# Kernel tuning notes

Measured on AMD Instinct MI355X. Metric: run time of the kernel, lower is better.

The kernel has to match this reference:

```python
import jax, jax.numpy as jnp
import numpy as np

# ---- hyperparameters (from init_kwargs) ----
W_KL = 1.0
W_AUX = 0.1
W_TRANS = 0.5
KL_FREE_BITS = 0.5
DIST_GAMMA = 1.0
FOCAL_GAMMA = 2.0
FOCAL_ALPHA = 0.6
SDTW_GAMMA = 0.1
BANDWIDTH = 150
BIG = 1e8  # finite 'infinity' so softmin gradients stay nan-free


def _focal_manhattan_cost(x, y):
    """Pairwise focal-weighted Manhattan distance.
    x: (B,N,D), y: (B,M,D) -> (B,N,M).
    d = dist_gamma * L1(x_i, y_j); focal weight alpha*(1-exp(-d))**focal_gamma.
    """
    d = DIST_GAMMA * jnp.abs(x[:, :, None, :] - y[:, None, :, :]).sum(-1)  # (B,N,M)
    w = FOCAL_ALPHA * (1.0 - jnp.exp(-d)) ** FOCAL_GAMMA
    return w * d


def _soft_dtw(x, y):
    """Banded Soft-DTW via anti-diagonal wavefront scan. x,y: (B,T,D) -> (B,)."""
    C = _focal_manhattan_cost(x, y)  # (B,T,T)
    B, T, _ = C.shape
    ii = jnp.arange(T + 1)  # padded row index i in [0,T]

    def _shift(a):  # a[:, i] -> a[:, i-1], pad with BIG
        return jnp.concatenate([jnp.full((a.shape[0], 1), BIG, a.dtype), a[:, :-1]], axis=1)

    def step(carry, d):
        prev2, prev = carry  # diagonals d-2, d-1; shape (B, T+1) indexed by i
        jj = d - ii
        valid = (ii >= 1) & (ii <= T) & (jj >= 1) & (jj <= T) & (jnp.abs(ii - jj) <= BANDWIDTH)
        ci = jnp.clip(ii - 1, 0, T - 1)
        cj = jnp.clip(jj - 1, 0, T - 1)
        cost = C[:, ci, cj]                     # (B, T+1) diagonal of cost matrix
        up = _shift(prev)                        # R[i-1, j]
        left = prev                              # R[i, j-1]
        diag = _shift(prev2)                     # R[i-1, j-1]
        stacked = jnp.stack([up, left, diag])    # (3, B, T+1)
        smin = -SDTW_GAMMA * jax.nn.logsumexp(stacked / (-SDTW_GAMMA), axis=0)
        r = jnp.where(valid, cost + smin, BIG)
        return (prev, r), None

    # d=0 diagonal: R[0,0]=0; d=1 diagonal: all boundary = BIG
    prev2 = jnp.full((B, T + 1), BIG, C.dtype).at[:, 0].set(0.0)
    prev = jnp.full((B, T + 1), BIG, C.dtype)
    (_, last), _ = jax.lax.scan(step, (prev2, prev), jnp.arange(2, 2 * T + 1))
    return last[:, T]  # R[T,T]


def _loss(pred_traj, ground_truth, style_mu, style_logvar, pred_trans_count, perm_gen, perm_real):
    # NAG loss: average Hausdorff (symmetric soft-DTW) + variation term
    sim = _soft_dtw(pred_traj, ground_truth).mean() + _soft_dtw(ground_truth, pred_traj).mean()
    d_gen = _soft_dtw(pred_traj, pred_traj[perm_gen]).mean()
    d_real = _soft_dtw(ground_truth, ground_truth[perm_real]).mean()
    nag = sim + jnp.abs(d_gen - d_real)

    # KL with free bits
    kl_div = -0.5 * jnp.sum(1.0 + style_logvar - style_mu ** 2 - jnp.exp(style_logvar), axis=1)
    kl = jnp.maximum(kl_div - KL_FREE_BITS, 0.0).mean()

    # transition counts
    gt_touch = ground_truth[..., 2]
    gt_trans = jnp.abs(gt_touch[:, 1:] - gt_touch[:, :-1]).sum(axis=1)  # hard count
    aux = jnp.mean((pred_trans_count.squeeze(-1) - gt_trans) ** 2)
    sharp = jax.nn.sigmoid((pred_traj[..., 2] - 0.5) * 10.0)
    pred_trans_soft = jnp.abs(sharp[:, 1:] - sharp[:, :-1]).sum(axis=1)
    trans_reg = jnp.mean((pred_trans_soft - gt_trans) ** 2)

    total = nag + W_KL * kl + W_AUX * aux + W_TRANS * trans_reg
    return total, nag, kl, aux, trans_reg


def setup_inputs() -> dict:
    key = jax.random.key(0)
    ks = jax.random.split(key, 7)
    B, T, D, L = 128, 256, 3, 128
    return {
        "pred_traj": jax.random.uniform(ks[0], (B, T, D), jnp.float32),
        "ground_truth": jax.random.uniform(ks[1], (B, T, D), jnp.float32),
        "style_mu": jax.random.normal(ks[2], (B, L), jnp.float32),
        "style_logvar": jax.random.normal(ks[3], (B, L), jnp.float32),
        "pred_trans_count": jax.random.normal(ks[4], (B, 1), jnp.float32),
        "perm_gen": jax.random.permutation(ks[5], B),
        "perm_real": jax.random.permutation(ks[6], B),
    }


def reference(pred_traj, ground_truth, style_mu, style_logvar, pred_trans_count, perm_gen, perm_real):
    return _loss(pred_traj, ground_truth, style_mu, style_logvar, pred_trans_count, perm_gen, perm_real)
```

## Files before the change

### kernel.cpp

```cpp
#include <hip/hip_runtime.h>

#define Tn 256
#define UBIG (-1.442695e9f)
#define CBIG (-3.0e9f)
#define E2(v)  __builtin_amdgcn_exp2f(v)

__global__ __launch_bounds__(256) void sdtw_kernel(
    const float* __restrict__ pred, const float* __restrict__ gt,
    const float* __restrict__ mu, const float* __restrict__ lv,
    const float* __restrict__ ptc,
    const int* __restrict__ perm_gen, const int* __restrict__ perm_real,
    float* __restrict__ ws) {
  __shared__ float ylds[Tn][3];
  __shared__ float rng[3][512];
  __shared__ volatile int prog[4];
  __shared__ float red[256];
  __shared__ float gtr_sh;

  const int t = threadIdx.x;

  if (blockIdx.x >= 384) {
    const int b = blockIdx.x - 384;

    float v = 0.0f;
    if (t < 128) {
      const float m = mu[b * 128 + t];
      const float l = lv[b * 128 + t];
      v = 1.0f + l - m * m - E2(l * 1.44269504f);
    }
    red[t] = v; __syncthreads();
    for (int s = 128; s > 0; s >>= 1) { if (t < s) red[t] += red[t + s]; __syncthreads(); }
    if (t == 0) ws[512 + b] = fmaxf(-0.5f * red[0] - 0.5f, 0.0f);
    __syncthreads();

    float g = 0.0f;
    if (t < Tn - 1)
      g = fabsf(gt[(b * Tn + t + 1) * 3 + 2] - gt[(b * Tn + t) * 3 + 2]);
    red[t] = g; __syncthreads();
    for (int s = 128; s > 0; s >>= 1) { if (t < s) red[t] += red[t + s]; __syncthreads(); }
    if (t == 0) gtr_sh = red[0];
    __syncthreads();
    const float gtr = gtr_sh;

    float p = 0.0f;
    if (t < Tn - 1) {
      const float q0 = pred[(b * Tn + t) * 3 + 2];
      const float q1 = pred[(b * Tn + t + 1) * 3 + 2];
      const float s0 = __builtin_amdgcn_rcpf(1.f + E2((q0 - 0.5f) * -14.4269504f));
      const float s1 = __builtin_amdgcn_rcpf(1.f + E2((q1 - 0.5f) * -14.4269504f));
      p = fabsf(s1 - s0);
    }
    red[t] = p; __syncthreads();
    for (int s = 128; s > 0; s >>= 1) { if (t < s) red[t] += red[t + s]; __syncthreads(); }
    if (t == 0) {
      const float pts = red[0];
      const float d1 = ptc[b] - gtr; ws[640 + b] = d1 * d1;
      const float d2 = pts - gtr;    ws[768 + b] = d2 * d2;
    }
    return;
  }

  const int blk = blockIdx.x;
  const int c = blk >> 7;
  const int b = blk & 127;

  const float* x;
  const float* y;
  if (c == 0)      { x = pred + b * Tn * 3; y = gt   + b * Tn * 3; }
  else if (c == 1) { x = pred + b * Tn * 3; y = pred + perm_gen[b]  * Tn * 3; }
  else             { x = gt   + b * Tn * 3; y = gt   + perm_real[b] * Tn * 3; }

  const int w = t >> 6;
  const int lane = t & 63;
  float* rngf = (float*)&rng[0][0];

  if (w == 0)      __builtin_amdgcn_s_setprio(3);
  else if (w == 1) __builtin_amdgcn_s_setprio(2);
  else if (w == 2) __builtin_amdgcn_s_setprio(1);

  for (int k = t; k < Tn * 3; k += 256) (&ylds[0][0])[k] = y[k] * 1.44269504f;
  for (int k = t; k < 3 * 512; k += 256) rngf[k] = UBIG;
  if (t < 4) prog[t] = 0;

  const float x0 = x[t * 3 + 0] * 1.44269504f;
  const float x1 = x[t * 3 + 1] * 1.44269504f;
  const float x2 = x[t * 3 + 2] * 1.44269504f;

  const int i = t + 1;
  const int lo = max(i + 1, 2 * i - 150);
  const int hi = min(i + Tn, 2 * i + 150);
  const unsigned span = (unsigned)(hi - lo);

  const int dstart = (w == 0) ? 2 : (w == 1) ? 66 : (w == 2) ? 130 : 225;
  const int dend   = (w == 0) ? 290 : (w == 1) ? 386 : (w == 2) ? 450 : 513;
  const bool wlt3 = (w != 3);

  int cjb = dstart - t - 2;
  int vdb = dstart - lo;

  __syncthreads();

  float lf = UBIG;
  float dgv;
  if (w > 0) {
    const int need0 = dstart - 2;
    int pv = prog[w - 1];
    while (pv < need0) { __builtin_amdgcn_s_sleep(1); pv = prog[w - 1]; }
    int gi = (w - 1) * 512 + dstart - 2;
    __asm__ volatile("" : "+v"(gi) : "v"(pv));
    const float r0 = rngf[gi];
    dgv = (lane == 0) ? r0 : UBIG;
  } else {
    dgv = (lane == 0) ? 0.0f : UBIG;
  }

#define COSTV(IDX, VD) ({                                                \
    const int cj_ = (IDX) & 255;                                         \
    const float a0 = x0 - ylds[cj_][0];                                  \
    const float a1 = x1 - ylds[cj_][1];                                  \
    const float a2 = x2 - ylds[cj_][2];                                  \
    const float dl_ = fabsf(a0) + fabsf(a1) + fabsf(a2);                 \
    const float om_ = 1.0f - E2(-dl_);                                   \
    const float cv_ = fmaf(om_ * dl_, -6.0f * om_, -127.0f);             \
    ((unsigned)(VD) <= span) ? cv_ : CBIG; })

  float cc[16], cn[16];
  #pragma unroll
  for (int k = 0; k < 16; ++k) cc[k] = COSTV(cjb + k, vdb + k);

  for (int dbase = dstart; dbase < dend; dbase += 16) {
    float bb[16];
    if (w > 0) {
      const int need = dbase + 14;
      int pv = prog[w - 1];
      while (pv < need) { __builtin_amdgcn_s_sleep(1); pv = prog[w - 1]; }
      int gb = (w - 1) * 512 + dbase - 1;
      __asm__ volatile("" : "+v"(gb) : "v"(pv));
      #pragma unroll
      for (int k = 0; k < 16; ++k) bb[k] = rngf[gb + k];
    } else {
      #pragma unroll
      for (int k = 0; k < 16; ++k) bb[k] = UBIG;
    }

    float rr[16];
    #pragma unroll
    for (int k = 0; k < 16; ++k) {
      const float upv = __int_as_float(__builtin_amdgcn_update_dpp(
          __float_as_int(bb[k]), __float_as_int(lf),
          0x138 , 0xf, 0xf, false));

      const float mx = fmaxf(fmaxf(upv, lf), dgv);
      const float md = __builtin_amdgcn_fmed3f(upv, lf, dgv);
      const float mn = fminf(fminf(upv, lf), dgv);
      const float fa = fmaf(md - mx, 8388608.0f, 1065353216.0f);
      const float fb = fmaf(mn - mx, 8388608.0f, 1065353216.0f);
      int ia, ib;
      __asm__("v_cvt_i32_f32 %0, %1" : "=v"(ia) : "v"(fa));
      __asm__("v_cvt_i32_f32 %0, %1" : "=v"(ib) : "v"(fb));
      const float s  = 1.0f + __int_as_float(ia) + __int_as_float(ib);
      const float fs = (float)__float_as_int(s);
      const float un = fmaf(fs, 1.1920928955e-7f, mx + cc[k]);
      rr[k] = un;
      dgv = upv;
      lf = un;
    }

    if (wlt3 && lane == 63) {
      #pragma unroll
      for (int k = 0; k < 16; ++k) rngf[w * 512 + dbase + k] = rr[k];
      prog[w] = dbase + 15;
    }

    #pragma unroll
    for (int k = 0; k < 16; ++k) cn[k] = COSTV(cjb + 16 + k, vdb + 16 + k);

    #pragma unroll
    for (int k = 0; k < 16; ++k) cc[k] = cn[k];
    cjb += 16;
    vdb += 16;
  }

  if (wlt3 && lane == 63) prog[w] = 0x7fffffff;

  if (t == 255) ws[blk] = lf * -0.0693147181f;
#undef COSTV
}

__global__ __launch_bounds__(128) void final_kernel(
    const float* __restrict__ ws, float* __restrict__ out) {
  const int t = threadIdx.x;
  __shared__ float red[128];
  const int offs[6] = {0, 128, 256, 512, 640, 768};
  float sums[6];
  #pragma unroll
  for (int q = 0; q < 6; ++q) {
    red[t] = ws[offs[q] + t];
    __syncthreads();
    for (int s = 64; s > 0; s >>= 1) { if (t < s) red[t] += red[t + s]; __syncthreads(); }
    if (t == 0) sums[q] = red[0];
    __syncthreads();
  }
  if (t == 0) {
    const float inv = 1.0f / 128.0f;
    const float sim   = 2.0f * sums[0] * inv;
    const float dgen  = sums[1] * inv;
    const float dreal = sums[2] * inv;
    const float nag   = sim + fabsf(dgen - dreal);
    const float kl    = sums[3] * inv;
    const float aux   = sums[4] * inv;
    const float trans = sums[5] * inv;
    const float total = nag + 1.0f * kl + 0.1f * aux + 0.5f * trans;
    out[0] = total;
    out[1] = nag;
    out[2] = kl;
    out[3] = aux;
    out[4] = trans;
  }
}

extern "C" void kernel_launch(void* const* d_in, const int* in_sizes, int n_in,
                              void* d_out, int out_size, void* d_ws, size_t ws_size,
                              hipStream_t stream) {
  const float* pred = (const float*)d_in[0];
  const float* gt   = (const float*)d_in[1];
  const float* mu   = (const float*)d_in[2];
  const float* lv   = (const float*)d_in[3];
  const float* ptc  = (const float*)d_in[4];
  const int*   pg   = (const int*)d_in[5];
  const int*   pr   = (const int*)d_in[6];
  float* ws  = (float*)d_ws;
  float* out = (float*)d_out;

  sdtw_kernel<<<512, 256, 0, stream>>>(pred, gt, mu, lv, ptc, pg, pr, ws);
  final_kernel<<<1, 128, 0, stream>>>(ws, out);
}
```

Before: 79.45 us.

## Double-buffer wavefront boundary loads and cost prefetch, use float4 LDS layout

Measured after the change: 70.77 us (median of 2 runs). -10.9%, faster.

```diff
diff --git a/kernel.cpp b/kernel.cpp
--- a/kernel.cpp
+++ b/kernel.cpp
@@ -4,6 +4,7 @@
 #define UBIG (-1.442695e9f)
 #define CBIG (-3.0e9f)
 #define E2(v)  __builtin_amdgcn_exp2f(v)
+#define L2E 1.44269504f
 
 __global__ __launch_bounds__(256) void sdtw_kernel(
     const float* __restrict__ pred, const float* __restrict__ gt,
@@ -11,8 +12,8 @@
     const float* __restrict__ ptc,
     const int* __restrict__ perm_gen, const int* __restrict__ perm_real,
     float* __restrict__ ws) {
-  __shared__ float ylds[Tn][3];
-  __shared__ float rng[3][512];
+  __shared__ float4 ylds4[640];
+  __shared__ float rng[3][520];
   __shared__ volatile int prog[4];
   __shared__ float red[256];
   __shared__ float gtr_sh;
@@ -26,7 +27,7 @@
     if (t < 128) {
       const float m = mu[b * 128 + t];
       const float l = lv[b * 128 + t];
-      v = 1.0f + l - m * m - E2(l * 1.44269504f);
+      v = 1.0f + l - m * m - E2(l * L2E);
     }
     red[t] = v; __syncthreads();
     for (int s = 128; s > 0; s >>= 1) { if (t < s) red[t] += red[t + s]; __syncthreads(); }
@@ -78,113 +79,129 @@
   else if (w == 1) __builtin_amdgcn_s_setprio(2);
   else if (w == 2) __builtin_amdgcn_s_setprio(1);
 
-  for (int k = t; k < Tn * 3; k += 256) (&ylds[0][0])[k] = y[k] * 1.44269504f;
-  for (int k = t; k < 3 * 512; k += 256) rngf[k] = UBIG;
+  for (int k = t; k < 640; k += 256) {
+    const int row = (k & 255) * 3;
+    ylds4[k] = float4{y[row] * L2E, y[row + 1] * L2E, y[row + 2] * L2E, 0.f};
+  }
+  for (int k = t; k < 3 * 520; k += 256) rngf[k] = UBIG;
   if (t < 4) prog[t] = 0;
 
-  const float x0 = x[t * 3 + 0] * 1.44269504f;
-  const float x1 = x[t * 3 + 1] * 1.44269504f;
-  const float x2 = x[t * 3 + 2] * 1.44269504f;
+  const float x0 = x[t * 3 + 0] * L2E;
+  const float x1 = x[t * 3 + 1] * L2E;
+  const float x2 = x[t * 3 + 2] * L2E;
 
   const int i = t + 1;
   const int lo = max(i + 1, 2 * i - 150);
   const int hi = min(i + Tn, 2 * i + 150);
   const unsigned span = (unsigned)(hi - lo);
 
-  const int dstart = (w == 0) ? 2 : (w == 1) ? 66 : (w == 2) ? 130 : 225;
-  const int dend   = (w == 0) ? 290 : (w == 1) ? 386 : (w == 2) ? 450 : 513;
+  const int dstart = (w == 0) ? 2 : (w == 1) ? 66 : (w == 2) ? 130 : 226;
+  const int dend   = (w == 0) ? 290 : (w == 1) ? 386 : (w == 2) ? 450 : 514;
   const bool wlt3 = (w != 3);
-
-  int cjb = dstart - t - 2;
-  int vdb = dstart - lo;
 
   __syncthreads();
 
   float lf = UBIG;
   float dgv;
+  float bbA[16], bbB[16], ccA[16], ccB[16];
+  int pvn = 0;
+
   if (w > 0) {
-    const int need0 = dstart - 2;
+    const int need0 = dstart + 14;
     int pv = prog[w - 1];
     while (pv < need0) { __builtin_amdgcn_s_sleep(1); pv = prog[w - 1]; }
-    int gi = (w - 1) * 512 + dstart - 2;
-    __asm__ volatile("" : "+v"(gi) : "v"(pv));
-    const float r0 = rngf[gi];
+    int gb = (w - 1) * 520 + dstart - 2;
+    __asm__ volatile("" : "+v"(gb) : "v"(pv));
+    const float r0 = rngf[gb];
     dgv = (lane == 0) ? r0 : UBIG;
+    #pragma unroll
+    for (int k = 0; k < 16; ++k) bbA[k] = rngf[gb + 1 + k];
+    pvn = prog[w - 1];
   } else {
     dgv = (lane == 0) ? 0.0f : UBIG;
-  }
-
-#define COSTV(IDX, VD) ({                                                \
-    const int cj_ = (IDX) & 255;                                         \
-    const float a0 = x0 - ylds[cj_][0];                                  \
-    const float a1 = x1 - ylds[cj_][1];                                  \
-    const float a2 = x2 - ylds[cj_][2];                                  \
-    const float dl_ = fabsf(a0) + fabsf(a1) + fabsf(a2);                 \
-    const float om_ = 1.0f - E2(-dl_);                                   \
-    const float cv_ = fmaf(om_ * dl_, -6.0f * om_, -127.0f);             \
-    ((unsigned)(VD) <= span) ? cv_ : CBIG; })
-
-  float cc[16], cn[16];
-  #pragma unroll
-  for (int k = 0; k < 16; ++k) cc[k] = COSTV(cjb + k, vdb + k);
-
-  for (int dbase = dstart; dbase < dend; dbase += 16) {
-    float bb[16];
-    if (w > 0) {
-      const int need = dbase + 14;
-      int pv = prog[w - 1];
-      while (pv < need) { __builtin_amdgcn_s_sleep(1); pv = prog[w - 1]; }
-      int gb = (w - 1) * 512 + dbase - 1;
-      __asm__ volatile("" : "+v"(gb) : "v"(pv));
-      #pragma unroll
-      for (int k = 0; k < 16; ++k) bb[k] = rngf[gb + k];
-    } else {
-      #pragma unroll
-      for (int k = 0; k < 16; ++k) bb[k] = UBIG;
-    }
-
-    float rr[16];
     #pragma unroll
-    for (int k = 0; k < 16; ++k) {
-      const float upv = __int_as_float(__builtin_amdgcn_update_dpp(
-          __float_as_int(bb[k]), __float_as_int(lf),
-          0x138 , 0xf, 0xf, false));
-
-      const float mx = fmaxf(fmaxf(upv, lf), dgv);
-      const float md = __builtin_amdgcn_fmed3f(upv, lf, dgv);
-      const float mn = fminf(fminf(upv, lf), dgv);
-      const float fa = fmaf(md - mx, 8388608.0f, 1065353216.0f);
-      const float fb = fmaf(mn - mx, 8388608.0f, 1065353216.0f);
-      int ia, ib;
-      __asm__("v_cvt_i32_f32 %0, %1" : "=v"(ia) : "v"(fa));
-      __asm__("v_cvt_i32_f32 %0, %1" : "=v"(ib) : "v"(fb));
-      const float s  = 1.0f + __int_as_float(ia) + __int_as_float(ib);
-      const float fs = (float)__float_as_int(s);
-      const float un = fmaf(fs, 1.1920928955e-7f, mx + cc[k]);
-      rr[k] = un;
-      dgv = upv;
-      lf = un;
-    }
-
-    if (wlt3 && lane == 63) {
-      #pragma unroll
-      for (int k = 0; k < 16; ++k) rngf[w * 512 + dbase + k] = rr[k];
-      prog[w] = dbase + 15;
-    }
-
-    #pragma unroll
-    for (int k = 0; k < 16; ++k) cn[k] = COSTV(cjb + 16 + k, vdb + 16 + k);
-
-    #pragma unroll
-    for (int k = 0; k < 16; ++k) cc[k] = cn[k];
-    cjb += 16;
-    vdb += 16;
+    for (int k = 0; k < 16; ++k) { bbA[k] = UBIG; bbB[k] = UBIG; }
+  }
+
+#define PREF16(CCX, DB) do {                                               \
+    const int sb_ = (DB) - t + 254;                                        \
+    const int vd_ = (DB) - lo;                                             \
+    _Pragma("unroll")                                                      \
+    for (int k_ = 0; k_ < 16; ++k_) {                                      \
+      const float4 yv_ = ylds4[sb_ + k_];                                  \
+      const float dl_ = fabsf(x0 - yv_.x) + fabsf(x1 - yv_.y) + fabsf(x2 - yv_.z); \
+      const float ef_ = fmaf(dl_, -8388608.f, 1065353216.f);               \
+      const float e_  = __int_as_float((int)ef_);                          \
+      const float om_ = 1.f - e_;                                          \
+      const float cv_ = fmaf(om_ * dl_, -6.f * om_, -127.f);               \
+      CCX[k_] = ((unsigned)(vd_ + k_) <= span) ? cv_ : CBIG;               \
+    } } while (0)
+
+#define CORE16(BBX, CCX, DB) do {                                          \
+    float rr_[16];                                                         \
+    _Pragma("unroll")                                                      \
+    for (int k_ = 0; k_ < 16; ++k_) {                                      \
+      const float upv_ = __int_as_float(__builtin_amdgcn_update_dpp(       \
+          __float_as_int(BBX[k_]), __float_as_int(lf),                     \
+          0x138 , 0xf, 0xf, false));                         \
+      float mx_, mn_;                                                      \
+      __asm__("v_max3_f32 %0, %1, %2, %3" : "=v"(mx_) : "v"(upv_), "v"(lf), "v"(dgv)); \
+      const float md_ = __builtin_amdgcn_fmed3f(upv_, lf, dgv);            \
+      __asm__("v_min3_f32 %0, %1, %2, %3" : "=v"(mn_) : "v"(upv_), "v"(lf), "v"(dgv)); \
+      const float fa_ = fmaf(md_ - mx_, 8388608.f, 1065353216.f);          \
+      const float fb_ = fmaf(mn_ - mx_, 8388608.f, 1065353216.f);          \
+      int ia_, ib_;                                                        \
+      __asm__("v_cvt_i32_f32 %0, %1" : "=v"(ia_) : "v"(fa_));              \
+      __asm__("v_cvt_i32_f32 %0, %1" : "=v"(ib_) : "v"(fb_));              \
+      const float s_ = 1.0f + __int_as_float(ia_) + __int_as_float(ib_);   \
+      const float fs_ = (float)__float_as_int(s_);                         \
+      const float un_ = fmaf(fs_, 1.1920928955e-7f, mx_ + CCX[k_]);        \
+      rr_[k_] = un_; dgv = upv_; lf = un_;                                 \
+    }                                                                      \
+    if (wlt3 && lane == 63) {                                              \
+      _Pragma("unroll")                                                    \
+      for (int k_ = 0; k_ < 16; ++k_) rngf[w * 520 + (DB) + k_] = rr_[k_]; \
+      prog[w] = (DB) + 15;                                                 \
+    }                                                                      \
+    res = rr_[14];                                                         \
+  } while (0)
+
+#define LOADBB(BBX, DB) do {                                               \
+    if (w > 0) {                                                           \
+      const int need_ = (DB) + 14;                                         \
+      if (pvn < need_) {                                                   \
+        int pv_ = prog[w - 1];                                             \
+        while (pv_ < need_) { __builtin_amdgcn_s_sleep(1); pv_ = prog[w - 1]; } \
+        pvn = pv_;                                                         \
+      }                                                                    \
+      int gb_ = (w - 1) * 520 + (DB) - 1;                                  \
+      __asm__ volatile("" : "+v"(gb_) : "v"(pvn));                         \
+      _Pragma("unroll")                                                    \
+      for (int k_ = 0; k_ < 16; ++k_) BBX[k_] = rngf[gb_ + k_];            \
+      pvn = prog[w - 1];                                                   \
+    } } while (0)
+
+  float res = UBIG;
+  PREF16(ccA, dstart);
+  #pragma unroll 1
+  for (int db = dstart; db < dend; db += 32) {
+    CORE16(bbA, ccA, db);
+    LOADBB(bbB, db + 16);
+    PREF16(ccB, db + 16);
+    CORE16(bbB, ccB, db + 16);
+    const bool more = (db + 32) < dend;
+    if (more) {
+      LOADBB(bbA, db + 32);
+      PREF16(ccA, db + 32);
+    }
   }
 
   if (wlt3 && lane == 63) prog[w] = 0x7fffffff;
 
-  if (t == 255) ws[blk] = lf * -0.0693147181f;
-#undef COSTV
+  if (t == 255) ws[blk] = res * -0.0693147181f;
+#undef PREF16
+#undef CORE16
+#undef LOADBB
 }
 
 __global__ __launch_bounds__(128) void final_kernel(
```
